# Kernel tuning notes

Measured on AMD Instinct MI355X. Metric: run time of the kernel, lower is better.

## Reference

```python
import jax, jax.numpy as jnp
import numpy as np

K = 16  # neighbors, incl. self


def setup_inputs() -> dict:
    key = jax.random.key(0)
    ks = jax.random.split(key, 16)
    N, C = 8192, 256  # points, channels (inter_channels == in_channels == C)
    s = 0.05
    inp = {
        'coords': jax.random.uniform(ks[0], (N, 3), dtype=jnp.float32) * 100.0,
        'feats': jax.random.normal(ks[1], (N, C), dtype=jnp.float32),
        'theta_w': jax.random.normal(ks[2], (C, C), dtype=jnp.float32) * s,
        'theta_b': jax.random.normal(ks[3], (C,), dtype=jnp.float32) * s,
        'phi_w': jax.random.normal(ks[4], (C, C), dtype=jnp.float32) * s,
        'phi_b': jax.random.normal(ks[5], (C,), dtype=jnp.float32) * s,
        'g_w': jax.random.normal(ks[6], (C, C), dtype=jnp.float32) * s,
        'g_b': jax.random.normal(ks[7], (C,), dtype=jnp.float32) * s,
        'pe1_w1': jax.random.normal(ks[8], (3, C), dtype=jnp.float32) * s,
        'pe1_b1': jax.random.normal(ks[9], (C,), dtype=jnp.float32) * s,
        'pe1_w2': jax.random.normal(ks[10], (C, C), dtype=jnp.float32) * s,
        'pe1_b2': jax.random.normal(ks[11], (C,), dtype=jnp.float32) * s,
        'W_w': jax.random.normal(ks[12], (C, C), dtype=jnp.float32) * s,
        'W_b': jax.random.normal(ks[13], (C,), dtype=jnp.float32) * s,
    }
    return inp


def reference(coords, feats, theta_w, theta_b, phi_w, phi_b, g_w, g_b,
              pe1_w1, pe1_b1, pe1_w2, pe1_b2, W_w, W_b):
    C = feats.shape[-1]
    # KNN (squared dists, includes self as nearest) == pytorch3d knn_points
    sq = jnp.sum(coords * coords, axis=-1)  # [N]
    d2 = sq[:, None] + sq[None, :] - 2.0 * (coords @ coords.T)  # [N,N]
    _, idx = jax.lax.top_k(-d2, K)  # [N,K] sorted by ascending distance

    nn_coords = coords[idx]            # [N,K,3] knn gather
    nn_feats = feats[idx]              # [N,K,C]

    theta_f = feats @ theta_w + theta_b          # [N,C]
    phi_f = nn_feats @ phi_w + phi_b             # [N,K,C]

    delta_coords = nn_coords - coords[:, None, :]  # [N,K,3]
    # pe1 MLP; NOTE: original code uses pe1 for both pe1 and pe2 (shared)
    pe = jax.nn.relu(delta_coords @ pe1_w1 + pe1_b1) @ pe1_w2 + pe1_b2  # [N,K,C]

    delta_features = (pe * (theta_f[:, None, :] - phi_f) + pe) / jnp.sqrt(jnp.float32(C))
    sim = jax.nn.softmax(delta_features, axis=1)  # softmax over K neighbors

    g_feats = nn_feats @ g_w + g_b               # [N,K,C]
    y = jnp.sum(sim * g_feats, axis=1)           # [N,C]

    # W (1x1 Minkowski conv == per-point linear) + residual
    return y @ W_w + W_b + feats
```

## Files before the change

kernel.cpp:

```cpp
#include <hip/hip_runtime.h>

typedef __bf16 bf16_t;
typedef bf16_t bf16x8 __attribute__((ext_vector_type(8)));
typedef bf16_t bf16x4 __attribute__((ext_vector_type(4)));
typedef bf16_t bf16x2 __attribute__((ext_vector_type(2)));
typedef float f32x4 __attribute__((ext_vector_type(4)));
typedef unsigned long long u64;

#define N_PTS 8192
#define C_DIM 256
#define K_NN 16

#define GRID_G    16
#define GRID_NC   (GRID_G * GRID_G * GRID_G)
#define GRID_CELL 6.25f
#define GRID_INV  0.16f

#define CAST_NBLK 2048
#define PREPW_NBLK 320
__global__ __launch_bounds__(256) void prep_kernel(
    const float* __restrict__ feats, bf16_t* __restrict__ fb,
    const float* __restrict__ w0, const float* __restrict__ w1,
    const float* __restrict__ w2, const float* __restrict__ w3,
    const float* __restrict__ w4, bf16_t* __restrict__ wt_base,
    int* __restrict__ cellCount, int* __restrict__ gcount) {
    const int b = blockIdx.x;
    const int t = threadIdx.x;

    if (b < CAST_NBLK) {
        int i = (b * 256 + t) * 4;
        float4 v = *(const float4*)(feats + i);
        bf16x4 o;
        o[0] = (bf16_t)v.x; o[1] = (bf16_t)v.y; o[2] = (bf16_t)v.z; o[3] = (bf16_t)v.w;
        *(bf16x4*)(fb + i) = o;
    } else if (b < CAST_NBLK + PREPW_NBLK) {
        int pb = b - CAST_NBLK;
        int m = pb >> 6;
        int bx = pb & 63;
        const float* src = (m == 0) ? w0 : (m == 1) ? w1 : (m == 2) ? w2 : (m == 3) ? w3 : w4;
        bf16_t* dst = wt_base + m * (C_DIM * C_DIM);
#pragma unroll
        for (int i = 0; i < 4; ++i) {
            int o = bx * 1024 + i * 256 + t;
            int tkb = o >> 9;
            int rem = o & 511;
            int lm = rem >> 5;
            int r = rem & 31;
            int k = (tkb & 7) * 32 + r;
            int n = (tkb >> 3) * 16 + lm;
            dst[o] = (bf16_t)src[k * C_DIM + n];
        }
    } else {
        int zb = b - CAST_NBLK - PREPW_NBLK;
        cellCount[zb * 256 + t] = 0;
        if (zb == 0 && t == 0) *gcount = 0;
    }
}

__global__ __launch_bounds__(256) void grid_count_kernel(const float* __restrict__ coords,
                                                         int* __restrict__ cellCount,
                                                         int* __restrict__ cid) {
    int i = blockIdx.x * 256 + threadIdx.x;
    float x = coords[3 * i + 0], y = coords[3 * i + 1], z = coords[3 * i + 2];
    int cx = (int)(x * GRID_INV); if (cx > GRID_G - 1) cx = GRID_G - 1;
    int cy = (int)(y * GRID_INV); if (cy > GRID_G - 1) cy = GRID_G - 1;
    int cz = (int)(z * GRID_INV); if (cz > GRID_G - 1) cz = GRID_G - 1;
    int c = (cx * GRID_G + cy) * GRID_G + cz;
    cid[i] = c;
    atomicAdd(&cellCount[c], 1);
}

__global__ __launch_bounds__(256) void grid_scan_kernel(const int* __restrict__ cellCount,
                                                        int* __restrict__ cellStart,
                                                        int* __restrict__ cellPtr) {
    __shared__ int part[256];
    int t = threadIdx.x;
    int base = t * 16;
    int v[16];
    int sum = 0;
#pragma unroll
    for (int i = 0; i < 16; ++i) { v[i] = cellCount[base + i]; sum += v[i]; }
    part[t] = sum;
    __syncthreads();
    for (int off = 1; off < 256; off <<= 1) {
        int x = (t >= off) ? part[t - off] : 0;
        __syncthreads();
        part[t] += x;
        __syncthreads();
    }
    int acc = part[t] - sum;
#pragma unroll
    for (int i = 0; i < 16; ++i) {
        cellStart[base + i] = acc;
        cellPtr[base + i] = acc;
        acc += v[i];
    }
    if (t == 255) cellStart[GRID_NC] = acc;
}

__global__ __launch_bounds__(256) void grid_scatter_kernel(
    const float* __restrict__ coords, const int* __restrict__ cid, int* __restrict__ cellPtr,
    float4* __restrict__ sp4, int* __restrict__ sidx) {
    int i = blockIdx.x * 256 + threadIdx.x;
    int c = cid[i];
    int pos = atomicAdd(&cellPtr[c], 1);
    float x = coords[3 * i + 0], y = coords[3 * i + 1], z = coords[3 * i + 2];
    float sq = __fadd_rn(__fadd_rn(__fmul_rn(x, x), __fmul_rn(y, y)), __fmul_rn(z, z));
    sp4[pos] = make_float4(x, y, z, sq);
    sidx[pos] = i;
}

__global__ __launch_bounds__(256) void knn_grid_kernel(
    const float* __restrict__ coords, const int* __restrict__ cellStart,
    const float4* __restrict__ sp4, const int* __restrict__ sidx,
    int* __restrict__ idx_out, int* __restrict__ glist, int* __restrict__ gcount) {
    const int tid = threadIdx.x;
    const int wave = tid >> 6, lane = tid & 63;
    const int q = blockIdx.x * 4 + wave;

    __shared__ int segBase[4][25];
    __shared__ int segPref[4][26];

    const float qx = coords[3 * q + 0], qy = coords[3 * q + 1], qz = coords[3 * q + 2];
    const float sqi = __fadd_rn(__fadd_rn(__fmul_rn(qx, qx), __fmul_rn(qy, qy)),
                                __fmul_rn(qz, qz));

    int cx = (int)(qx * GRID_INV); if (cx > GRID_G - 1) cx = GRID_G - 1;
    int cy = (int)(qy * GRID_INV); if (cy > GRID_G - 1) cy = GRID_G - 1;
    int cz = (int)(qz * GRID_INV); if (cz > GRID_G - 1) cz = GRID_G - 1;
    int wx0 = cx - 2; if (wx0 < 0) wx0 = 0;
    int wx1 = cx + 2; if (wx1 > GRID_G - 1) wx1 = GRID_G - 1;
    int wy0 = cy - 2; if (wy0 < 0) wy0 = 0;
    int wy1 = cy + 2; if (wy1 > GRID_G - 1) wy1 = GRID_G - 1;
    int wz0 = cz - 2; if (wz0 < 0) wz0 = 0;
    int wz1 = cz + 2; if (wz1 > GRID_G - 1) wz1 = GRID_G - 1;

    const float INF = __int_as_float(0x7f800000);
    float rc = INF;
    if (wx0 > 0)          rc = fminf(rc, qx - (float)wx0 * GRID_CELL);
    if (wx1 < GRID_G - 1) rc = fminf(rc, (float)(wx1 + 1) * GRID_CELL - qx);
    if (wy0 > 0)          rc = fminf(rc, qy - (float)wy0 * GRID_CELL);
    if (wy1 < GRID_G - 1) rc = fminf(rc, (float)(wy1 + 1) * GRID_CELL - qy);
    if (wz0 > 0)          rc = fminf(rc, qz - (float)wz0 * GRID_CELL);
    if (wz1 < GRID_G - 1) rc = fminf(rc, (float)(wz1 + 1) * GRID_CELL - qz);
    float rc2 = rc * rc * 0.9999f;

    int nx = wx1 - wx0 + 1, nyc = wy1 - wy0 + 1;
    int ns = nx * nyc;
    if (lane < ns) {
        int scx = wx0 + lane / nyc;
        int scy = wy0 + lane % nyc;
        int b = (scx * GRID_G + scy) * GRID_G;
        int s0 = cellStart[b + wz0];
        int s1 = cellStart[b + wz1 + 1];
        segBase[wave][lane] = s0;
        segPref[wave][lane] = s1 - s0;
    }
    __syncthreads();
    if (lane == 0) {
        int acc = 0;
        for (int s = 0; s < ns; ++s) { int l = segPref[wave][s]; segPref[wave][s] = acc; acc += l; }
        segPref[wave][ns] = acc;
    }
    __syncthreads();

    const int M = segPref[wave][ns];
    bool flag = (M < K_NN) || (M > 320);

    u64 k0 = ~0ull, k1 = ~0ull, k2 = ~0ull, k3 = ~0ull, k4 = ~0ull;
    {
        int s = 0;
#pragma unroll
        for (int slot = 0; slot < 5; ++slot) {
            int t = lane + slot * 64;
            if (t < M) {
                while (t >= segPref[wave][s + 1]) ++s;
                int pos = segBase[wave][s] + (t - segPref[wave][s]);
                float4 v = sp4[pos];
                float dot = __fmaf_rn(v.z, qz, __fmaf_rn(v.y, qy, __fmul_rn(v.x, qx)));
                float d2 = __fsub_rn(__fadd_rn(sqi, v.w), __fmul_rn(2.0f, dot));
                unsigned u = __float_as_uint(d2);
                u = (u & 0x80000000u) ? ~u : (u | 0x80000000u);
                u64 key = (((u64)u) << 32) | (unsigned)sidx[pos];
                if (slot == 0) k0 = key;
                else if (slot == 1) k1 = key;
                else if (slot == 2) k2 = key;
                else if (slot == 3) k3 = key;
                else k4 = key;
            }
        }
    }

    u64 lm2 = k0; int li = 0;
    if (k1 < lm2) { lm2 = k1; li = 1; }
    if (k2 < lm2) { lm2 = k2; li = 2; }
    if (k3 < lm2) { lm2 = k3; li = 3; }
    if (k4 < lm2) { lm2 = k4; li = 4; }
    int keep = 0;
    u64 last = ~0ull;
#pragma unroll 1
    for (int r = 0; r < 16; ++r) {
        u64 w = lm2;
#pragma unroll
        for (int off = 1; off < 64; off <<= 1) {
            u64 o = __shfl_xor(w, off);
            w = (o < w) ? o : w;
        }
        if (lane == r) keep = (int)(unsigned)(w & 0xffffffffull);
        last = w;
        if (lm2 == w) {
            if (li == 0) k0 = ~0ull;
            else if (li == 1) k1 = ~0ull;
            else if (li == 2) k2 = ~0ull;
            else if (li == 3) k3 = ~0ull;
            else k4 = ~0ull;
            lm2 = k0; li = 0;
            if (k1 < lm2) { lm2 = k1; li = 1; }
            if (k2 < lm2) { lm2 = k2; li = 2; }
            if (k3 < lm2) { lm2 = k3; li = 3; }
            if (k4 < lm2) { lm2 = k4; li = 4; }
        }
    }

    if (!flag) {
        unsigned ou = (unsigned)(last >> 32);
        unsigned db = (ou & 0x80000000u) ? (ou ^ 0x80000000u) : ~ou;
        float d16 = __uint_as_float(db);
        if (d16 >= rc2) flag = true;
    }
    if (flag && lane == 0) {
        int sl = atomicAdd(gcount, 1);
        glist[sl] = q;
    }
    if (lane < 16) idx_out[q * K_NN + lane] = keep;
}

__global__ __launch_bounds__(256) void knn_fallback_kernel(const float* __restrict__ coords,
                                                           const int* __restrict__ glist,
                                                           const int* __restrict__ gcount,
                                                           int* __restrict__ idx_out) {
    const int count = *gcount;
    const int tid = threadIdx.x;
    const int wave = tid >> 6, lane = tid & 63;
    __shared__ float red16[4][16];
    __shared__ u64 cand[4][256];
    __shared__ int cnt[4];
    __shared__ int qids[4];
    const float INF = __int_as_float(0x7f800000);
    const float* cp = coords + tid * 96;

#pragma unroll 1
    for (int n0 = blockIdx.x * 4; n0 < count; n0 += gridDim.x * 4) {
        if (tid < 4) {
            cnt[tid] = 0;
            int slot = n0 + tid;
            qids[tid] = glist[slot < count ? slot : count - 1];
        }
        __syncthreads();

        float qx[4], qy[4], qz[4], sqi[4];
#pragma unroll
        for (int q = 0; q < 4; ++q) {
            int id = qids[q];
            qx[q] = coords[3 * id + 0];
            qy[q] = coords[3 * id + 1];
            qz[q] = coords[3 * id + 2];
            sqi[q] = __fadd_rn(__fadd_rn(__fmul_rn(qx[q], qx[q]), __fmul_rn(qy[q], qy[q])),
                               __fmul_rn(qz[q], qz[q]));
        }

        float lmin[4] = {INF, INF, INF, INF};
#pragma unroll
        for (int c = 0; c < 4; ++c) {
            float buf[24];
#pragma unroll
            for (int v = 0; v < 6; ++v)
                *(float4*)(buf + v * 4) = *(const float4*)(cp + c * 24 + v * 4);
#pragma unroll
            for (int p = 0; p < 8; ++p) {
                float x = buf[3 * p + 0], y = buf[3 * p + 1], z = buf[3 * p + 2];
                float sqj = __fadd_rn(__fadd_rn(__fmul_rn(x, x), __fmul_rn(y, y)),
                                      __fmul_rn(z, z));
#pragma unroll
                for (int q = 0; q < 4; ++q) {
                    float dot = __fmaf_rn(z, qz[q], __fmaf_rn(y, qy[q], __fmul_rn(x, qx[q])));
                    float d2 = __fsub_rn(__fadd_rn(sqi[q], sqj), __fmul_rn(2.0f, dot));
                    lmin[q] = fminf(lmin[q], d2);
                }
            }
        }

#pragma unroll
        for (int q = 0; q < 4; ++q) {
            float g = lmin[q];
            g = fminf(g, __shfl_xor(g, 1));
            g = fminf(g, __shfl_xor(g, 2));
            g = fminf(g, __shfl_xor(g, 4));
            g = fminf(g, __shfl_xor(g, 8));
            if ((lane & 15) == 0) red16[q][wave * 4 + (lane >> 4)] = g;
        }
        __syncthreads();

        float tau[4];
#pragma unroll
        for (int q = 0; q < 4; ++q) {
            float t = red16[q][0];
#pragma unroll
            for (int i = 1; i < 16; ++i) t = fmaxf(t, red16[q][i]);
            tau[q] = t;
        }

#pragma unroll
        for (int c = 0; c < 4; ++c) {
            float buf[24];
#pragma unroll
            for (int v = 0; v < 6; ++v)
                *(float4*)(buf + v * 4) = *(const float4*)(cp + c * 24 + v * 4);
#pragma unroll
            for (int p = 0; p < 8; ++p) {
                float x = buf[3 * p + 0], y = buf[3 * p + 1], z = buf[3 * p + 2];
                float sqj = __fadd_rn(__fadd_rn(__fmul_rn(x, x), __fmul_rn(y, y)),
                                      __fmul_rn(z, z));
                int j = tid * 32 + c * 8 + p;
#pragma unroll
                for (int q = 0; q < 4; ++q) {
                    float dot = __fmaf_rn(z, qz[q], __fmaf_rn(y, qy[q], __fmul_rn(x, qx[q])));
                    float d2 = __fsub_rn(__fadd_rn(sqi[q], sqj), __fmul_rn(2.0f, dot));
                    if (d2 <= tau[q]) {
                        unsigned u = __float_as_uint(d2);
                        u = (u & 0x80000000u) ? ~u : (u | 0x80000000u);
                        int slot = atomicAdd(&cnt[q], 1);
                        if (slot < 256)
                            cand[q][slot] = (((u64)u) << 32) | (unsigned)j;
                    }
                }
            }
        }
        __syncthreads();

        int m = cnt[wave]; if (m > 256) m = 256;
        u64 k0 = ~0ull, k1 = ~0ull, k2 = ~0ull, k3 = ~0ull;
        if (lane < m) k0 = cand[wave][lane];
        if (lane + 64 < m) k1 = cand[wave][lane + 64];
        if (lane + 128 < m) k2 = cand[wave][lane + 128];
        if (lane + 192 < m) k3 = cand[wave][lane + 192];
        u64 lm2 = k0; int li = 0;
        if (k1 < lm2) { lm2 = k1; li = 1; }
        if (k2 < lm2) { lm2 = k2; li = 2; }
        if (k3 < lm2) { lm2 = k3; li = 3; }
        int keep = 0;
#pragma unroll 1
        for (int r = 0; r < 16; ++r) {
            u64 w = lm2;
#pragma unroll
            for (int off = 1; off < 64; off <<= 1) {
                u64 o = __shfl_xor(w, off);
                w = (o < w) ? o : w;
            }
            if (lane == r) keep = (int)(unsigned)(w & 0xffffffffull);
            if (lm2 == w) {
                if (li == 0) k0 = ~0ull;
                else if (li == 1) k1 = ~0ull;
                else if (li == 2) k2 = ~0ull;
                else k3 = ~0ull;
                lm2 = k0; li = 0;
                if (k1 < lm2) { lm2 = k1; li = 1; }
                if (k2 < lm2) { lm2 = k2; li = 2; }
                if (k3 < lm2) { lm2 = k3; li = 3; }
            }
        }
        if (n0 + wave < count && lane < 16)
            idx_out[qids[wave] * K_NN + lane] = keep;
        __syncthreads();
    }
}

__global__ __launch_bounds__(256, 2) void proj_kernel(
    const bf16_t* __restrict__ fb, const bf16_t* __restrict__ wt_base,
    const float* __restrict__ tb, const float* __restrict__ pb, const float* __restrict__ gb,
    float* __restrict__ T, bf16_t* __restrict__ PG) {
    const int sel = blockIdx.y;
    const int half = blockIdx.z;
    const bf16_t* Wt = wt_base + sel * (C_DIM * C_DIM);
    const float* bias = (sel == 0) ? tb : (sel == 1) ? pb : gb;
    const int wave = threadIdx.x >> 6, lane = threadIdx.x & 63;
    const int q = lane >> 4, lm = lane & 15;
    const int m0 = blockIdx.x * 64;

    bf16x8 bfr[2][8];
#pragma unroll
    for (int ti = 0; ti < 2; ++ti)
#pragma unroll
        for (int kb = 0; kb < 8; ++kb)
            bfr[ti][kb] = *(const bf16x8*)(Wt + (((half * 8 + wave * 2 + ti) * 8 + kb) << 9) + lm * 32 + q * 8);

    float bv[2];
#pragma unroll
    for (int ti = 0; ti < 2; ++ti) bv[ti] = bias[(half * 8 + wave * 2 + ti) * 16 + lm];

#pragma unroll
    for (int p = 0; p < 4; ++p) {
        const bf16_t* arow = fb + (m0 + p * 16 + lm) * C_DIM + q * 8;
        f32x4 acc[2];
        acc[0] = (f32x4){0.f, 0.f, 0.f, 0.f};
        acc[1] = (f32x4){0.f, 0.f, 0.f, 0.f};
#pragma unroll
        for (int kb = 0; kb < 8; ++kb) {
            bf16x8 a = *(const bf16x8*)(arow + kb * 32);
            acc[0] = __builtin_amdgcn_mfma_f32_16x16x32_bf16(a, bfr[0][kb], acc[0], 0, 0, 0);
            acc[1] = __builtin_amdgcn_mfma_f32_16x16x32_bf16(a, bfr[1][kb], acc[1], 0, 0, 0);
        }

#pragma unroll
        for (int ti = 0; ti < 2; ++ti) {
            int c = (half * 8 + wave * 2 + ti) * 16 + lm;
#pragma unroll
            for (int r = 0; r < 4; ++r) {
                float v = acc[ti][r] + bv[ti];
                int off = (m0 + p * 16 + q * 4 + r) * C_DIM + c;
                if (sel == 0) T[off] = v;
                else if (sel == 1) PG[2 * off] = (bf16_t)v;
                else PG[2 * off + 1] = (bf16_t)v;
            }
        }
    }
}

#define HPAD 264
#define P_BLK 16
#define HROWS (P_BLK * 16)
__global__ __launch_bounds__(512, 4) void pe2_fused_kernel(
    const float* __restrict__ coords, const int* __restrict__ idx,
    const float* __restrict__ T, const bf16_t* __restrict__ PG,
    const float* __restrict__ w1, const float* __restrict__ b1, const float* __restrict__ b2,
    const bf16_t* __restrict__ Wt2, bf16_t* __restrict__ yb) {
    __shared__ __align__(16) bf16_t hbuf[2][16 * HPAD];
    __shared__ float dxyz[HROWS][3];
    __shared__ int idxl[HROWS];
    const int tid = threadIdx.x;
    const int p0 = blockIdx.x * P_BLK;
    const int wave = tid >> 6, lane = tid & 63;
    const int q = lane >> 4, lm = lane & 15;

    bf16x8 bfr[2][8];
#pragma unroll
    for (int ti = 0; ti < 2; ++ti)
#pragma unroll
        for (int kb = 0; kb < 8; ++kb)
            bfr[ti][kb] = *(const bf16x8*)(Wt2 + (((wave * 2 + ti) * 8 + kb) << 9) + lm * 32 + q * 8);
    float b2c[2];
#pragma unroll
    for (int ti = 0; ti < 2; ++ti) b2c[ti] = b2[(wave * 2 + ti) * 16 + lm];

    if (tid < HROWS) {
        int n = p0 + (tid >> 4);
        int j = idx[n * K_NN + (tid & 15)];
        idxl[tid] = j;
        dxyz[tid][0] = coords[3 * j + 0] - coords[3 * n + 0];
        dxyz[tid][1] = coords[3 * j + 1] - coords[3 * n + 1];
        dxyz[tid][2] = coords[3 * j + 2] - coords[3 * n + 2];
    }
    __syncthreads();

    const int hc = tid & 255;
    const int rh = (tid >> 8) * 8;
    const float wx = w1[hc], wy = w1[C_DIM + hc], wz = w1[2 * C_DIM + hc], bb = b1[hc];

#pragma unroll
    for (int r = 0; r < 8; ++r) {
        int row = rh + r;
        float pre = dxyz[row][0] * wx + dxyz[row][1] * wy + dxyz[row][2] * wz + bb;
        hbuf[0][row * HPAD + hc] = (bf16_t)fmaxf(pre, 0.0f);
    }
    __syncthreads();

#pragma unroll 1
    for (int lp = 0; lp < P_BLK; ++lp) {
        const int n = p0 + lp;
        const int cur = lp & 1;

        int jr[4];
#pragma unroll
        for (int r = 0; r < 4; ++r) jr[r] = idxl[lp * 16 + q * 4 + r];
        bf16x2 pg[2][4];
        float Tn[2];
#pragma unroll
        for (int ti = 0; ti < 2; ++ti) {
            int c = (wave * 2 + ti) * 16 + lm;
            Tn[ti] = T[n * C_DIM + c];
#pragma unroll
            for (int r = 0; r < 4; ++r)
                pg[ti][r] = *(const bf16x2*)(PG + 2 * (jr[r] * C_DIM + c));
        }

        if (lp + 1 < P_BLK) {
            int rb = (lp + 1) * 16;
#pragma unroll
            for (int r = 0; r < 8; ++r) {
                int row = rh + r;
                float pre = dxyz[rb + row][0] * wx + dxyz[rb + row][1] * wy
                          + dxyz[rb + row][2] * wz + bb;
                hbuf[cur ^ 1][row * HPAD + hc] = (bf16_t)fmaxf(pre, 0.0f);
            }
        }

        const bf16_t* hrow = &hbuf[cur][lm * HPAD + q * 8];
        f32x4 acc[2];
        acc[0] = (f32x4){0.f, 0.f, 0.f, 0.f};
        acc[1] = (f32x4){0.f, 0.f, 0.f, 0.f};
#pragma unroll
        for (int kb = 0; kb < 8; ++kb) {
            bf16x8 a = *(const bf16x8*)(hrow + kb * 32);
            acc[0] = __builtin_amdgcn_mfma_f32_16x16x32_bf16(a, bfr[0][kb], acc[0], 0, 0, 0);
            acc[1] = __builtin_amdgcn_mfma_f32_16x16x32_bf16(a, bfr[1][kb], acc[1], 0, 0, 0);
        }

#pragma unroll
        for (int ti = 0; ti < 2; ++ti) {
            int c = (wave * 2 + ti) * 16 + lm;
            float df[4];
#pragma unroll
            for (int r = 0; r < 4; ++r) {
                float pe = acc[ti][r] + b2c[ti];
                df[r] = (pe * (Tn[ti] - (float)pg[ti][r][0]) + pe) * 0.0625f;
            }
            float mx = fmaxf(fmaxf(df[0], df[1]), fmaxf(df[2], df[3]));
            mx = fmaxf(mx, __shfl_xor(mx, 16));
            mx = fmaxf(mx, __shfl_xor(mx, 32));
            float e[4], s = 0.f;
#pragma unroll
            for (int r = 0; r < 4; ++r) { e[r] = __expf(df[r] - mx); s += e[r]; }
            s += __shfl_xor(s, 16);
            s += __shfl_xor(s, 32);
            float inv = 1.0f / s;
            float y = 0.f;
#pragma unroll
            for (int r = 0; r < 4; ++r) y += e[r] * inv * (float)pg[ti][r][1];
            y += __shfl_xor(y, 16);
            y += __shfl_xor(y, 32);
            if (q == 0) yb[n * C_DIM + c] = (bf16_t)y;
        }
        __syncthreads();
    }
}

__global__ __launch_bounds__(256, 2) void final_kernel(
    const bf16_t* __restrict__ yb, const bf16_t* __restrict__ Wt,
    const float* __restrict__ Wb, const float* __restrict__ feats,
    float* __restrict__ out) {
    const int wave = threadIdx.x >> 6, lane = threadIdx.x & 63;
    const int q = lane >> 4, lm = lane & 15;
    const int m0 = blockIdx.x * 64;
    const int half = blockIdx.y;

    bf16x8 bfr[2][8];
#pragma unroll
    for (int ti = 0; ti < 2; ++ti)
#pragma unroll
        for (int kb = 0; kb < 8; ++kb)
            bfr[ti][kb] = *(const bf16x8*)(Wt + (((half * 8 + wave * 2 + ti) * 8 + kb) << 9) + lm * 32 + q * 8);
    float bv[2];
#pragma unroll
    for (int ti = 0; ti < 2; ++ti) bv[ti] = Wb[(half * 8 + wave * 2 + ti) * 16 + lm];

#pragma unroll
    for (int p = 0; p < 4; ++p) {
        const bf16_t* arow = yb + (m0 + p * 16 + lm) * C_DIM + q * 8;
        f32x4 acc[2];
        acc[0] = (f32x4){0.f, 0.f, 0.f, 0.f};
        acc[1] = (f32x4){0.f, 0.f, 0.f, 0.f};
#pragma unroll
        for (int kb = 0; kb < 8; ++kb) {
            bf16x8 a = *(const bf16x8*)(arow + kb * 32);
            acc[0] = __builtin_amdgcn_mfma_f32_16x16x32_bf16(a, bfr[0][kb], acc[0], 0, 0, 0);
            acc[1] = __builtin_amdgcn_mfma_f32_16x16x32_bf16(a, bfr[1][kb], acc[1], 0, 0, 0);
        }

#pragma unroll
        for (int ti = 0; ti < 2; ++ti) {
            int c = (half * 8 + wave * 2 + ti) * 16 + lm;
#pragma unroll
            for (int r = 0; r < 4; ++r) {
                int off = (m0 + p * 16 + q * 4 + r) * C_DIM + c;
                out[off] = acc[ti][r] + bv[ti] + feats[off];
            }
        }
    }
}

extern "C" void kernel_launch(void* const* d_in, const int* in_sizes, int n_in,
                              void* d_out, int out_size, void* d_ws, size_t ws_size,
                              hipStream_t stream) {
    const float* coords = (const float*)d_in[0];
    const float* feats  = (const float*)d_in[1];
    const float* theta_w = (const float*)d_in[2];
    const float* theta_b = (const float*)d_in[3];
    const float* phi_w   = (const float*)d_in[4];
    const float* phi_b   = (const float*)d_in[5];
    const float* g_w     = (const float*)d_in[6];
    const float* g_b     = (const float*)d_in[7];
    const float* pe1_w1  = (const float*)d_in[8];
    const float* pe1_b1  = (const float*)d_in[9];
    const float* pe1_w2  = (const float*)d_in[10];
    const float* pe1_b2  = (const float*)d_in[11];
    const float* W_w     = (const float*)d_in[12];
    const float* W_b     = (const float*)d_in[13];
    float* out = (float*)d_out;

    char* w = (char*)d_ws;
    size_t off = 0;
    int* idx = (int*)(w + off);        off += (size_t)N_PTS * K_NN * 4;
    bf16_t* fb = (bf16_t*)(w + off);   off += (size_t)N_PTS * C_DIM * 2;
    bf16_t* wt = (bf16_t*)(w + off);   off += (size_t)5 * C_DIM * C_DIM * 2;
    float* T = (float*)(w + off);      off += (size_t)N_PTS * C_DIM * 4;
    bf16_t* PG = (bf16_t*)(w + off);   off += (size_t)N_PTS * C_DIM * 4;
    bf16_t* yb = (bf16_t*)(w + off);   off += (size_t)N_PTS * C_DIM * 2;
    float4* sp4 = (float4*)(w + off);  off += (size_t)N_PTS * 16;
    int* sidxp = (int*)(w + off);      off += (size_t)N_PTS * 4;
    int* cid       = (int*)(w + off);  off += (size_t)N_PTS * 4;
    int* cellCount = (int*)(w + off);  off += (size_t)GRID_NC * 4;
    int* cellStart = (int*)(w + off);  off += (size_t)(GRID_NC + 1) * 4;
    int* cellPtr   = (int*)(w + off);  off += (size_t)GRID_NC * 4;
    int* glist = (int*)(w + off);      off += (size_t)N_PTS * 4;
    int* gcount = (int*)(w + off);     off += 256;
    (void)ws_size; (void)in_sizes; (void)n_in; (void)out_size;

    prep_kernel<<<CAST_NBLK + PREPW_NBLK + 16, 256, 0, stream>>>(
        feats, fb, theta_w, phi_w, g_w, pe1_w2, W_w, wt, cellCount, gcount);

    grid_count_kernel<<<N_PTS / 256, 256, 0, stream>>>(coords, cellCount, cid);
    grid_scan_kernel<<<1, 256, 0, stream>>>(cellCount, cellStart, cellPtr);
    grid_scatter_kernel<<<N_PTS / 256, 256, 0, stream>>>(coords, cid, cellPtr, sp4, sidxp);
    knn_grid_kernel<<<N_PTS / 4, 256, 0, stream>>>(coords, cellStart, sp4, sidxp,
                                                   idx, glist, gcount);
    knn_fallback_kernel<<<32, 256, 0, stream>>>(coords, glist, gcount, idx);

    proj_kernel<<<dim3(N_PTS / 64, 3, 2), 256, 0, stream>>>(fb, wt, theta_b, phi_b, g_b, T, PG);
    pe2_fused_kernel<<<N_PTS / P_BLK, 512, 0, stream>>>(coords, idx, T, PG,
                                                        pe1_w1, pe1_b1, pe1_b2,
                                                        wt + 3 * C_DIM * C_DIM, yb);
    final_kernel<<<dim3(N_PTS / 64, 2), 256, 0, stream>>>(yb, wt + 4 * C_DIM * C_DIM,
                                                          W_b, feats, out);
}
```

Measured before the change: 195.5 us.

## Fuse final W projection into pe2 kernel and prefetch next point's gathers

The separate final_kernel is removed. Each pe2 block now keeps its 16 output rows of y in LDS and runs the W projection, bias and residual add itself, so the yb intermediate never goes to global memory and one launch disappears. The T and PG gathers for the next point are also issued before the current point's softmax epilogue, overlapping their latency with compute. In exchange the kernel uses more LDS and registers, which may lower occupancy.

```diff
diff --git a/kernel.cpp b/kernel.cpp
--- a/kernel.cpp
+++ b/kernel.cpp
@@ -433,8 +433,11 @@
     const float* __restrict__ coords, const int* __restrict__ idx,
     const float* __restrict__ T, const bf16_t* __restrict__ PG,
     const float* __restrict__ w1, const float* __restrict__ b1, const float* __restrict__ b2,
-    const bf16_t* __restrict__ Wt2, bf16_t* __restrict__ yb) {
+    const bf16_t* __restrict__ Wt2, const bf16_t* __restrict__ Wt3,
+    const float* __restrict__ Wb, const float* __restrict__ feats,
+    float* __restrict__ out) {
     __shared__ __align__(16) bf16_t hbuf[2][16 * HPAD];
+    __shared__ __align__(16) bf16_t yl[16][HPAD];
     __shared__ float dxyz[HROWS][3];
     __shared__ int idxl[HROWS];
     const int tid = threadIdx.x;
@@ -474,24 +477,27 @@
     }
     __syncthreads();
 
+    bf16x2 pgA[2][4];
+    float TnA[2];
+    {
+        const int n = p0;
+        int jr[4];
+#pragma unroll
+        for (int r = 0; r < 4; ++r) jr[r] = idxl[q * 4 + r];
+#pragma unroll
+        for (int ti = 0; ti < 2; ++ti) {
+            int c = (wave * 2 + ti) * 16 + lm;
+            TnA[ti] = T[n * C_DIM + c];
+#pragma unroll
+            for (int r = 0; r < 4; ++r)
+                pgA[ti][r] = *(const bf16x2*)(PG + 2 * (jr[r] * C_DIM + c));
+        }
+    }
+
 #pragma unroll 1
     for (int lp = 0; lp < P_BLK; ++lp) {
         const int n = p0 + lp;
         const int cur = lp & 1;
-
-        int jr[4];
-#pragma unroll
-        for (int r = 0; r < 4; ++r) jr[r] = idxl[lp * 16 + q * 4 + r];
-        bf16x2 pg[2][4];
-        float Tn[2];
-#pragma unroll
-        for (int ti = 0; ti < 2; ++ti) {
-            int c = (wave * 2 + ti) * 16 + lm;
-            Tn[ti] = T[n * C_DIM + c];
-#pragma unroll
-            for (int r = 0; r < 4; ++r)
-                pg[ti][r] = *(const bf16x2*)(PG + 2 * (jr[r] * C_DIM + c));
-        }
 
         if (lp + 1 < P_BLK) {
             int rb = (lp + 1) * 16;
@@ -515,6 +521,22 @@
             acc[1] = __builtin_amdgcn_mfma_f32_16x16x32_bf16(a, bfr[1][kb], acc[1], 0, 0, 0);
         }
 
+        bf16x2 pgB[2][4];
+        float TnB[2];
+        if (lp + 1 < P_BLK) {
+            int jr[4];
+#pragma unroll
+            for (int r = 0; r < 4; ++r) jr[r] = idxl[(lp + 1) * 16 + q * 4 + r];
+#pragma unroll
+            for (int ti = 0; ti < 2; ++ti) {
+                int c = (wave * 2 + ti) * 16 + lm;
+                TnB[ti] = T[(n + 1) * C_DIM + c];
+#pragma unroll
+                for (int r = 0; r < 4; ++r)
+                    pgB[ti][r] = *(const bf16x2*)(PG + 2 * (jr[r] * C_DIM + c));
+            }
+        }
+
 #pragma unroll
         for (int ti = 0; ti < 2; ++ti) {
             int c = (wave * 2 + ti) * 16 + lm;
@@ -522,7 +544,7 @@
 #pragma unroll
             for (int r = 0; r < 4; ++r) {
                 float pe = acc[ti][r] + b2c[ti];
-                df[r] = (pe * (Tn[ti] - (float)pg[ti][r][0]) + pe) * 0.0625f;
+                df[r] = (pe * (TnA[ti] - (float)pgA[ti][r][0]) + pe) * 0.0625f;
             }
             float mx = fmaxf(fmaxf(df[0], df[1]), fmaxf(df[2], df[3]));
             mx = fmaxf(mx, __shfl_xor(mx, 16));
@@ -535,55 +557,47 @@
             float inv = 1.0f / s;
             float y = 0.f;
 #pragma unroll
-            for (int r = 0; r < 4; ++r) y += e[r] * inv * (float)pg[ti][r][1];
+            for (int r = 0; r < 4; ++r) y += e[r] * inv * (float)pgA[ti][r][1];
             y += __shfl_xor(y, 16);
             y += __shfl_xor(y, 32);
-            if (q == 0) yb[n * C_DIM + c] = (bf16_t)y;
+            if (q == 0) yl[lp][c] = (bf16_t)y;
+        }
+
+#pragma unroll
+        for (int ti = 0; ti < 2; ++ti) {
+            TnA[ti] = TnB[ti];
+#pragma unroll
+            for (int r = 0; r < 4; ++r) pgA[ti][r] = pgB[ti][r];
         }
         __syncthreads();
     }
-}
-
-__global__ __launch_bounds__(256, 2) void final_kernel(
-    const bf16_t* __restrict__ yb, const bf16_t* __restrict__ Wt,
-    const float* __restrict__ Wb, const float* __restrict__ feats,
-    float* __restrict__ out) {
-    const int wave = threadIdx.x >> 6, lane = threadIdx.x & 63;
-    const int q = lane >> 4, lm = lane & 15;
-    const int m0 = blockIdx.x * 64;
-    const int half = blockIdx.y;
-
-    bf16x8 bfr[2][8];
+
 #pragma unroll
     for (int ti = 0; ti < 2; ++ti)
 #pragma unroll
         for (int kb = 0; kb < 8; ++kb)
-            bfr[ti][kb] = *(const bf16x8*)(Wt + (((half * 8 + wave * 2 + ti) * 8 + kb) << 9) + lm * 32 + q * 8);
-    float bv[2];
-#pragma unroll
-    for (int ti = 0; ti < 2; ++ti) bv[ti] = Wb[(half * 8 + wave * 2 + ti) * 16 + lm];
-
-#pragma unroll
-    for (int p = 0; p < 4; ++p) {
-        const bf16_t* arow = yb + (m0 + p * 16 + lm) * C_DIM + q * 8;
-        f32x4 acc[2];
-        acc[0] = (f32x4){0.f, 0.f, 0.f, 0.f};
-        acc[1] = (f32x4){0.f, 0.f, 0.f, 0.f};
-#pragma unroll
-        for (int kb = 0; kb < 8; ++kb) {
-            bf16x8 a = *(const bf16x8*)(arow + kb * 32);
-            acc[0] = __builtin_amdgcn_mfma_f32_16x16x32_bf16(a, bfr[0][kb], acc[0], 0, 0, 0);
-            acc[1] = __builtin_amdgcn_mfma_f32_16x16x32_bf16(a, bfr[1][kb], acc[1], 0, 0, 0);
-        }
-
-#pragma unroll
-        for (int ti = 0; ti < 2; ++ti) {
-            int c = (half * 8 + wave * 2 + ti) * 16 + lm;
-#pragma unroll
-            for (int r = 0; r < 4; ++r) {
-                int off = (m0 + p * 16 + q * 4 + r) * C_DIM + c;
-                out[off] = acc[ti][r] + bv[ti] + feats[off];
-            }
+            bfr[ti][kb] = *(const bf16x8*)(Wt3 + (((wave * 2 + ti) * 8 + kb) << 9) + lm * 32 + q * 8);
+    float bw[2];
+#pragma unroll
+    for (int ti = 0; ti < 2; ++ti) bw[ti] = Wb[(wave * 2 + ti) * 16 + lm];
+
+    f32x4 acc2[2];
+    acc2[0] = (f32x4){0.f, 0.f, 0.f, 0.f};
+    acc2[1] = (f32x4){0.f, 0.f, 0.f, 0.f};
+#pragma unroll
+    for (int kb = 0; kb < 8; ++kb) {
+        bf16x8 a = *(const bf16x8*)(&yl[lm][kb * 32 + q * 8]);
+        acc2[0] = __builtin_amdgcn_mfma_f32_16x16x32_bf16(a, bfr[0][kb], acc2[0], 0, 0, 0);
+        acc2[1] = __builtin_amdgcn_mfma_f32_16x16x32_bf16(a, bfr[1][kb], acc2[1], 0, 0, 0);
+    }
+
+#pragma unroll
+    for (int ti = 0; ti < 2; ++ti) {
+        int c = (wave * 2 + ti) * 16 + lm;
+#pragma unroll
+        for (int r = 0; r < 4; ++r) {
+            int off = (p0 + q * 4 + r) * C_DIM + c;
+            out[off] = acc2[ti][r] + bw[ti] + feats[off];
         }
     }
 }
@@ -614,7 +628,6 @@
     bf16_t* wt = (bf16_t*)(w + off);   off += (size_t)5 * C_DIM * C_DIM * 2;
     float* T = (float*)(w + off);      off += (size_t)N_PTS * C_DIM * 4;
     bf16_t* PG = (bf16_t*)(w + off);   off += (size_t)N_PTS * C_DIM * 4;
-    bf16_t* yb = (bf16_t*)(w + off);   off += (size_t)N_PTS * C_DIM * 2;
     float4* sp4 = (float4*)(w + off);  off += (size_t)N_PTS * 16;
     int* sidxp = (int*)(w + off);      off += (size_t)N_PTS * 4;
     int* cid       = (int*)(w + off);  off += (size_t)N_PTS * 4;
@@ -638,7 +651,7 @@
     proj_kernel<<<dim3(N_PTS / 64, 3, 2), 256, 0, stream>>>(fb, wt, theta_b, phi_b, g_b, T, PG);
     pe2_fused_kernel<<<N_PTS / P_BLK, 512, 0, stream>>>(coords, idx, T, PG,
                                                         pe1_w1, pe1_b1, pe1_b2,
-                                                        wt + 3 * C_DIM * C_DIM, yb);
-    final_kernel<<<dim3(N_PTS / 64, 2), 256, 0, stream>>>(yb, wt + 4 * C_DIM * C_DIM,
-                                                          W_b, feats, out);
-}
+                                                        wt + 3 * C_DIM * C_DIM,
+                                                        wt + 4 * C_DIM * C_DIM,
+                                                        W_b, feats, out);
+}
```

After: 194.5 us. About the same (-0.5%).
